# Kernel optimization log

Hardware: AMD Instinct MI355X
Metric: run time of the kernel (lower is better)

Reference implementation:

```python
import jax, jax.numpy as jnp
import numpy as np

D_MODEL = 1024
NUM_HEADS = 16
HEAD_DIM = D_MODEL // NUM_HEADS


def setup_inputs() -> dict:
    key = jax.random.key(0)
    ks = jax.random.split(key, 9)
    s = 1.0 / np.sqrt(D_MODEL)
    x = jax.random.normal(ks[0], (2, 2048, D_MODEL), dtype=jnp.float32)
    Wq = jax.random.normal(ks[1], (D_MODEL, D_MODEL), dtype=jnp.float32) * s
    Wk = jax.random.normal(ks[2], (D_MODEL, D_MODEL), dtype=jnp.float32) * s
    Wv = jax.random.normal(ks[3], (D_MODEL, D_MODEL), dtype=jnp.float32) * s
    Wo = jax.random.normal(ks[4], (D_MODEL, D_MODEL), dtype=jnp.float32) * s
    bq = jax.random.normal(ks[5], (D_MODEL,), dtype=jnp.float32) * s
    bk = jax.random.normal(ks[6], (D_MODEL,), dtype=jnp.float32) * s
    bv = jax.random.normal(ks[7], (D_MODEL,), dtype=jnp.float32) * s
    bo = jax.random.normal(ks[8], (D_MODEL,), dtype=jnp.float32) * s
    return {"x": x, "Wq": Wq, "bq": bq, "Wk": Wk, "bk": bk, "Wv": Wv, "bv": bv, "Wo": Wo, "bo": bo}


def reference(x, Wq, bq, Wk, bk, Wv, bv, Wo, bo):
    B, S, D = x.shape
    H, Hd = NUM_HEADS, HEAD_DIM
    # QKV projections
    q = (x @ Wq + bq).reshape(B, S, H, Hd).transpose(0, 2, 1, 3)  # [B,H,S,Hd]
    k = (x @ Wk + bk).reshape(B, S, H, Hd).transpose(0, 2, 1, 3)
    v = (x @ Wv + bv).reshape(B, S, H, Hd).transpose(0, 2, 1, 3)
    scores = jnp.einsum("bhqd,bhkd->bhqk", q, k) / jnp.sqrt(jnp.float32(Hd))
    attn = jax.nn.softmax(scores, axis=-1)
    out = jnp.einsum("bhqk,bhkd->bhqd", attn, v)  # [B,H,S,Hd]
    out = out.transpose(0, 2, 1, 3).reshape(B, S, D)
    return out @ Wo + bo
```

## Files before the change

kernel.cpp:

```cpp
#include <hip/hip_runtime.h>
#include <hip/hip_bf16.h>


typedef unsigned short u16;

#define D_MODEL 1024
#define NHEAD 16
#define HDIM 64
#define BATCH 2
#define SEQ 2048
#define MTOT (BATCH * SEQ)

#define QSCALE 0.18033688011112042f

using frag_ab = __attribute__((ext_vector_type(8))) short;
using frag_s4 = __attribute__((ext_vector_type(4))) short;
using frag_cd = __attribute__((ext_vector_type(4))) float;

__device__ __forceinline__ u16 f2u(float f) {
    union { float f; unsigned int i; } x;
    x.f = f;
    unsigned int r = x.i + 0x7fffu + ((x.i >> 16) & 1u);
    return (u16)(r >> 16);
}
__device__ __forceinline__ unsigned int pkrn(float a, float b) {
    union { __hip_bfloat162 h; unsigned int u; } c;
    c.h = __float22bfloat162_rn(float2{a, b});
    return c.u;
}

__global__ void prep(const float* __restrict__ W0, const float* __restrict__ W1,
                     const float* __restrict__ W2, const float* __restrict__ W3,
                     const float* __restrict__ X, u16* __restrict__ Wt,
                     u16* __restrict__ Xb) {
    const int z = blockIdx.z;
    const int tx = threadIdx.x, ty = threadIdx.y;
    if (z < 4) {
        __shared__ u16 t[32][33];
        const float* W = (z == 0) ? W0 : (z == 1) ? W1 : (z == 2) ? W2 : W3;
        u16* o = Wt + (size_t)z * D_MODEL * D_MODEL;
        int n0 = blockIdx.x * 32, k0 = blockIdx.y * 32;
        #pragma unroll
        for (int i = ty; i < 32; i += 8) t[i][tx] = f2u(W[(size_t)(k0 + i) * D_MODEL + n0 + tx]);
        __syncthreads();
        #pragma unroll
        for (int i = ty; i < 32; i += 8) o[(size_t)(n0 + i) * D_MODEL + k0 + tx] = t[tx][i];
    } else {
        int tid = ty * 32 + tx;
        size_t base = ((size_t)(blockIdx.y * 32 + blockIdx.x) * 256 + tid) * 16;
        #pragma unroll
        for (int c = 0; c < 4; ++c) {
            float4 v = *(const float4*)&X[base + c * 4];
            ushort4 o;
            o.x = f2u(v.x); o.y = f2u(v.y); o.z = f2u(v.z); o.w = f2u(v.w);
            *(ushort4*)&Xb[base + c * 4] = o;
        }
    }
}

__launch_bounds__(256, 3)
__global__ void gemm_qkvt(const u16* __restrict__ xb, const u16* __restrict__ Wt,
                          const float* __restrict__ bq, const float* __restrict__ bk,
                          const float* __restrict__ bv, u16* __restrict__ QKw,
                          u16* __restrict__ Vtw) {
    constexpr int BK = 64;
    __shared__ __attribute__((aligned(16))) u16 As[128 * BK];
    __shared__ __attribute__((aligned(16))) u16 Bs[128 * BK];

    const int tid = threadIdx.x;
    const int w = tid >> 6;
    const int lane = tid & 63;
    const int lrow = lane & 15, lquad = lane >> 4;
    const size_t WSZ = (size_t)D_MODEL * D_MODEL;

    const int bid = blockIdx.x;
    const bool vt = bid >= 512;
    const int z = vt ? 2 : (bid >> 8);
    const int t = vt ? (bid - 512) : (bid & 255);
    const int n0 = vt ? (t & 31) * 128 : (t & 7) * 128;
    const int m0 = vt ? (t >> 5) * 128 : (t >> 3) * 128;
    const u16* Ap = vt ? (Wt + 2 * WSZ) : xb;
    const u16* Bp = vt ? xb : (Wt + (size_t)z * WSZ);
    const float* bias = vt ? bv : (z ? bk : bq);

    frag_cd acc[4][4];
    #pragma unroll
    for (int i = 0; i < 4; i++)
        #pragma unroll
        for (int j = 0; j < 4; j++) acc[i][j] = (frag_cd){0.f, 0.f, 0.f, 0.f};

    const int wm = (w >> 1) * 64, wn = (w & 1) * 64;

    for (int k0 = 0; k0 < D_MODEL; k0 += BK) {
        __syncthreads();
        #pragma unroll
        for (int it = 0; it < 4; ++it) {
            int c = it * 256 + tid;
            int r = c >> 3, c8 = c & 7;
            const u16* ga = Ap + (size_t)(m0 + r) * D_MODEL + k0 + c8 * 8;
            char* la = (char*)As + (it * 256 + w * 64) * 16;
            __builtin_amdgcn_global_load_lds((const __attribute__((address_space(1))) void*)ga,
                                             (__attribute__((address_space(3))) void*)la, 16, 0, 0);
            const u16* gb = Bp + (size_t)(n0 + r) * D_MODEL + k0 + c8 * 8;
            char* lb = (char*)Bs + (it * 256 + w * 64) * 16;
            __builtin_amdgcn_global_load_lds((const __attribute__((address_space(1))) void*)gb,
                                             (__attribute__((address_space(3))) void*)lb, 16, 0, 0);
        }
        __syncthreads();

        #pragma unroll
        for (int kc = 0; kc < 2; ++kc) {
            frag_ab av[4], bvv[4];
            #pragma unroll
            for (int i = 0; i < 4; i++)
                av[i] = *(const frag_ab*)&As[(wm + i * 16 + lrow) * BK + kc * 32 + lquad * 8];
            #pragma unroll
            for (int j = 0; j < 4; j++)
                bvv[j] = *(const frag_ab*)&Bs[(wn + j * 16 + lrow) * BK + kc * 32 + lquad * 8];
            #pragma unroll
            for (int i = 0; i < 4; i++)
                #pragma unroll
                for (int j = 0; j < 4; j++)
                    acc[i][j] = __builtin_amdgcn_mfma_f32_16x16x32_bf16(av[i], bvv[j], acc[i][j], 0, 0, 0);
        }
    }

    const float scale = (!vt && z == 0) ? QSCALE : 1.0f;
    #pragma unroll
    for (int j = 0; j < 4; j++) {
        int gn = n0 + wn + j * 16 + lrow;
        #pragma unroll
        for (int i = 0; i < 4; i++) {
            #pragma unroll
            for (int rr = 0; rr < 4; ++rr) {
                int gm = m0 + wm + i * 16 + lquad * 4 + rr;
                if (!vt) {
                    float v = (acc[i][j][rr] + bias[gn]) * scale;
                    u16* oz = QKw + (size_t)z * ((size_t)MTOT * D_MODEL);
                    int b = gm >> 11, s = gm & (SEQ - 1);
                    int h = gn >> 6, d = gn & (HDIM - 1);
                    oz[(((size_t)(b * NHEAD + h)) * SEQ + s) * HDIM + d] = f2u(v);
                } else {
                    float v = acc[i][j][rr] + bias[gm];
                    int h = gm >> 6, d = gm & (HDIM - 1);
                    int b = gn >> 11, s = gn & (SEQ - 1);
                    Vtw[(((size_t)(b * NHEAD + h)) * HDIM + d) * SEQ + s] = f2u(v);
                }
            }
        }
    }
}

__launch_bounds__(256, 2)
__global__ void gemm_out(const u16* __restrict__ A, const u16* __restrict__ Wt,
                         const float* __restrict__ bias, float* __restrict__ out) {
    constexpr int BK = 64;
    __shared__ __attribute__((aligned(16))) u16 As[64 * BK];
    __shared__ __attribute__((aligned(16))) u16 Bs[128 * BK];

    const int tid = threadIdx.x;
    const int w = tid >> 6;
    const int lane = tid & 63;
    const int lrow = lane & 15, lquad = lane >> 4;
    const int m0 = blockIdx.y * 64, n0 = blockIdx.x * 128;

    frag_cd acc[2][4];
    #pragma unroll
    for (int i = 0; i < 2; i++)
        #pragma unroll
        for (int j = 0; j < 4; j++) acc[i][j] = (frag_cd){0.f, 0.f, 0.f, 0.f};

    const int wm = (w >> 1) * 32, wn = (w & 1) * 64;

    for (int k0 = 0; k0 < D_MODEL; k0 += BK) {
        __syncthreads();
        #pragma unroll
        for (int it = 0; it < 2; ++it) {
            int c = it * 256 + tid;
            int r = c >> 3, c8 = c & 7;
            const u16* ga = A + (size_t)(m0 + r) * D_MODEL + k0 + c8 * 8;
            char* la = (char*)As + (it * 256 + w * 64) * 16;
            __builtin_amdgcn_global_load_lds((const __attribute__((address_space(1))) void*)ga,
                                             (__attribute__((address_space(3))) void*)la, 16, 0, 0);
        }
        #pragma unroll
        for (int it = 0; it < 4; ++it) {
            int c = it * 256 + tid;
            int r = c >> 3, c8 = c & 7;
            const u16* gb = Wt + (size_t)(n0 + r) * D_MODEL + k0 + c8 * 8;
            char* lb = (char*)Bs + (it * 256 + w * 64) * 16;
            __builtin_amdgcn_global_load_lds((const __attribute__((address_space(1))) void*)gb,
                                             (__attribute__((address_space(3))) void*)lb, 16, 0, 0);
        }
        __syncthreads();

        #pragma unroll
        for (int kc = 0; kc < 2; ++kc) {
            frag_ab av[2], bvv[4];
            #pragma unroll
            for (int i = 0; i < 2; i++)
                av[i] = *(const frag_ab*)&As[(wm + i * 16 + lrow) * BK + kc * 32 + lquad * 8];
            #pragma unroll
            for (int j = 0; j < 4; j++)
                bvv[j] = *(const frag_ab*)&Bs[(wn + j * 16 + lrow) * BK + kc * 32 + lquad * 8];
            #pragma unroll
            for (int i = 0; i < 2; i++)
                #pragma unroll
                for (int j = 0; j < 4; j++)
                    acc[i][j] = __builtin_amdgcn_mfma_f32_16x16x32_bf16(av[i], bvv[j], acc[i][j], 0, 0, 0);
        }
    }

    #pragma unroll
    for (int j = 0; j < 4; j++) {
        int gn = n0 + wn + j * 16 + lrow;
        float bvf = bias[gn];
        #pragma unroll
        for (int i = 0; i < 2; i++)
            #pragma unroll
            for (int rr = 0; rr < 4; ++rr) {
                int gm = m0 + wm + i * 16 + lquad * 4 + rr;
                out[(size_t)gm * D_MODEL + gn] = acc[i][j][rr] + bvf;
            }
    }
}

__launch_bounds__(512, 4)
__global__ void attn_kernel(const u16* __restrict__ Q, const u16* __restrict__ K,
                            const u16* __restrict__ Vt, u16* __restrict__ O) {
    constexpr int SKK = 72;
    __shared__ __attribute__((aligned(16))) u16 Ks[128 * SKK];
    __shared__ __attribute__((aligned(16))) u16 Vs[64 * 128];

    const int tid = threadIdx.x;
    const int w = tid >> 6;
    const int lane = tid & 63;
    const int lrow = lane & 15, lquad = lane >> 4;
    const int bh = blockIdx.y;
    const int q0 = blockIdx.x * 128;
    const size_t base = (size_t)bh * SEQ * HDIM;
    const u16* Qg = Q + base;
    const u16* Kg = K + base;
    const u16* Vg = Vt + base;

    frag_ab qf[2];
    #pragma unroll
    for (int kc = 0; kc < 2; ++kc)
        qf[kc] = *(const frag_ab*)&Qg[(size_t)(q0 + w * 16 + lrow) * HDIM + kc * 32 + lquad * 8];

    frag_cd accOT[4];
    #pragma unroll
    for (int df = 0; df < 4; df++) accOT[df] = (frag_cd){0.f, 0.f, 0.f, 0.f};
    float lacc = 0.f;

    for (int kt = 0; kt < SEQ / 128; ++kt) {
        __syncthreads();
        #pragma unroll
        for (int it = 0; it < 2; ++it) {
            int c = it * 512 + tid;
            int rk = c >> 3, ck = (c & 7) * 8;
            *(uint4*)&Ks[rk * SKK + ck] = *(const uint4*)&Kg[(size_t)(kt * 128 + rk) * HDIM + ck];
            int rv = c >> 4, gv = c & 15;
            *(uint4*)&Vs[rv * 128 + ((gv ^ (rv & 7)) << 3)] =
                *(const uint4*)&Vg[(size_t)rv * SEQ + kt * 128 + gv * 8];
        }
        __syncthreads();

        frag_cd sc[8];
        #pragma unroll
        for (int mf = 0; mf < 8; mf++) sc[mf] = (frag_cd){0.f, 0.f, 0.f, 0.f};
        #pragma unroll
        for (int kc = 0; kc < 2; ++kc)
            #pragma unroll
            for (int mf = 0; mf < 8; mf++) {
                frag_ab kf = *(const frag_ab*)&Ks[(mf * 16 + lrow) * SKK + kc * 32 + lquad * 8];
                sc[mf] = __builtin_amdgcn_mfma_f32_16x16x32_bf16(kf, qf[kc], sc[mf], 0, 0, 0);
            }

        frag_s4 pk[8];
        #pragma unroll
        for (int mf = 0; mf < 8; mf++) {
            float e0 = exp2f(sc[mf][0]), e1 = exp2f(sc[mf][1]);
            float e2 = exp2f(sc[mf][2]), e3 = exp2f(sc[mf][3]);
            lacc += (e0 + e1) + (e2 + e3);
            union { frag_s4 s; unsigned int u[2]; } pu;
            pu.u[0] = pkrn(e0, e1);
            pu.u[1] = pkrn(e2, e3);
            pk[mf] = pu.s;
        }

        #pragma unroll
        for (int mf = 0; mf < 8; mf++)
            #pragma unroll
            for (int df = 0; df < 4; df++) {
                int dr = df * 16 + lrow;
                int g = 2 * mf + (lquad >> 1);
                frag_s4 vf = *(const frag_s4*)&Vs[dr * 128 + ((g ^ (dr & 7)) << 3) + (lquad & 1) * 4];
                accOT[df] = __builtin_amdgcn_mfma_f32_16x16x16bf16_1k(vf, pk[mf], accOT[df], 0, 0, 0);
            }
    }

    lacc += __shfl_xor(lacc, 16);
    lacc += __shfl_xor(lacc, 32);

    const int b = bh >> 4, h = bh & (NHEAD - 1);
    const int s = q0 + w * 16 + lrow;
    const float inv = 1.0f / lacc;
    u16* orow = O + ((size_t)(b * SEQ + s)) * D_MODEL + h * HDIM;
    #pragma unroll
    for (int df = 0; df < 4; df++) {
        union { unsigned int u[2]; ushort4 s4; } o;
        o.u[0] = pkrn(accOT[df][0] * inv, accOT[df][1] * inv);
        o.u[1] = pkrn(accOT[df][2] * inv, accOT[df][3] * inv);
        *(ushort4*)&orow[df * 16 + lquad * 4] = o.s4;
    }
}

extern "C" void kernel_launch(void* const* d_in, const int* in_sizes, int n_in,
                              void* d_out, int out_size, void* d_ws, size_t ws_size,
                              hipStream_t stream) {
    const float* x  = (const float*)d_in[0];
    const float* Wq = (const float*)d_in[1];
    const float* bq = (const float*)d_in[2];
    const float* Wk = (const float*)d_in[3];
    const float* bk = (const float*)d_in[4];
    const float* Wv = (const float*)d_in[5];
    const float* bv = (const float*)d_in[6];
    const float* Wo = (const float*)d_in[7];
    const float* bo = (const float*)d_in[8];

    u16* ws = (u16*)d_ws;
    const size_t WSZ = (size_t)D_MODEL * D_MODEL;
    const size_t TSZ = (size_t)MTOT * D_MODEL;
    u16* xb  = ws;
    u16* Wt  = ws + 4 * WSZ;
    u16* QKw = ws + 8 * WSZ;
    u16* Vtw = QKw + 2 * TSZ;
    u16* Aw  = Vtw + TSZ;

    prep<<<dim3(32, 32, 5), dim3(32, 8), 0, stream>>>(Wq, Wk, Wv, Wo, x, Wt, xb);
    gemm_qkvt<<<dim3(768), 256, 0, stream>>>(xb, Wt, bq, bk, bv, QKw, Vtw);
    attn_kernel<<<dim3(16, 32), 512, 0, stream>>>(QKw, QKw + TSZ, Vtw, Aw);
    gemm_out<<<dim3(8, 64), 256, 0, stream>>>(Aw, Wt + 3 * WSZ, bo, (float*)d_out);
}
```

Before: 220.4 us.

## Double-buffer K/V tiles in attention using async global-to-LDS loads

The attention kernel now keeps two LDS buffers for K and V. It prefetches the next key tile with direct global-to-LDS loads while the current tile feeds the MFMAs, and needs only one barrier per iteration instead of two. K moves from a padded layout to an XOR-swizzled layout so the direct-load lane mapping stays bank-conflict-free. The cost is doubled LDS per block (64KB), which may cut how many blocks fit on each CU.

```diff
diff --git a/kernel.cpp b/kernel.cpp
--- a/kernel.cpp
+++ b/kernel.cpp
@@ -228,9 +228,8 @@
 __launch_bounds__(512, 4)
 __global__ void attn_kernel(const u16* __restrict__ Q, const u16* __restrict__ K,
                             const u16* __restrict__ Vt, u16* __restrict__ O) {
-    constexpr int SKK = 72;
-    __shared__ __attribute__((aligned(16))) u16 Ks[128 * SKK];
-    __shared__ __attribute__((aligned(16))) u16 Vs[64 * 128];
+    __shared__ __attribute__((aligned(16))) u16 Ks[2][128 * 64];
+    __shared__ __attribute__((aligned(16))) u16 Vs[2][64 * 128];
 
     const int tid = threadIdx.x;
     const int w = tid >> 6;
@@ -253,29 +252,46 @@
     for (int df = 0; df < 4; df++) accOT[df] = (frag_cd){0.f, 0.f, 0.f, 0.f};
     float lacc = 0.f;
 
+    auto stage = [&](int bsel, int kt2) {
+        const u16* Kt = Kg + (size_t)(kt2 * 128) * HDIM;
+        #pragma unroll
+        for (int it = 0; it < 2; ++it) {
+            const int c = it * 512 + tid;
+            const int rk = c >> 3, ck = c & 7;
+            const u16* gk = Kt + rk * HDIM + ((ck ^ (rk & 7)) << 3);
+            char* lk = (char*)&Ks[bsel][0] + (it * 512 + w * 64) * 16;
+            __builtin_amdgcn_global_load_lds((const __attribute__((address_space(1))) void*)gk,
+                                             (__attribute__((address_space(3))) void*)lk, 16, 0, 0);
+            const int rv = c >> 4, gv = c & 15;
+            const u16* gvp = Vg + (size_t)rv * SEQ + kt2 * 128 + ((gv ^ (rv & 7)) << 3);
+            char* lv = (char*)&Vs[bsel][0] + (it * 512 + w * 64) * 16;
+            __builtin_amdgcn_global_load_lds((const __attribute__((address_space(1))) void*)gvp,
+                                             (__attribute__((address_space(3))) void*)lv, 16, 0, 0);
+        }
+    };
+
+    stage(0, 0);
+    __syncthreads();
+
+    int buf = 0;
     for (int kt = 0; kt < SEQ / 128; ++kt) {
-        __syncthreads();
-        #pragma unroll
-        for (int it = 0; it < 2; ++it) {
-            int c = it * 512 + tid;
-            int rk = c >> 3, ck = (c & 7) * 8;
-            *(uint4*)&Ks[rk * SKK + ck] = *(const uint4*)&Kg[(size_t)(kt * 128 + rk) * HDIM + ck];
-            int rv = c >> 4, gv = c & 15;
-            *(uint4*)&Vs[rv * 128 + ((gv ^ (rv & 7)) << 3)] =
-                *(const uint4*)&Vg[(size_t)rv * SEQ + kt * 128 + gv * 8];
-        }
-        __syncthreads();
+        if (kt + 1 < SEQ / 128) stage(buf ^ 1, kt + 1);
+
+        const u16* Ksb = &Ks[buf][0];
+        const u16* Vsb = &Vs[buf][0];
 
         frag_cd sc[8];
         #pragma unroll
         for (int mf = 0; mf < 8; mf++) sc[mf] = (frag_cd){0.f, 0.f, 0.f, 0.f};
         #pragma unroll
-        for (int kc = 0; kc < 2; ++kc)
+        for (int kc = 0; kc < 2; ++kc) {
+            const int cswz = (((kc << 2) + lquad) ^ (lrow & 7)) << 3;
             #pragma unroll
             for (int mf = 0; mf < 8; mf++) {
-                frag_ab kf = *(const frag_ab*)&Ks[(mf * 16 + lrow) * SKK + kc * 32 + lquad * 8];
+                frag_ab kf = *(const frag_ab*)&Ksb[(mf * 16 + lrow) * 64 + cswz];
                 sc[mf] = __builtin_amdgcn_mfma_f32_16x16x32_bf16(kf, qf[kc], sc[mf], 0, 0, 0);
             }
+        }
 
         frag_s4 pk[8];
         #pragma unroll
@@ -290,14 +306,18 @@
         }
 
         #pragma unroll
-        for (int mf = 0; mf < 8; mf++)
+        for (int mf = 0; mf < 8; mf++) {
+            const int g = 2 * mf + (lquad >> 1);
             #pragma unroll
             for (int df = 0; df < 4; df++) {
-                int dr = df * 16 + lrow;
-                int g = 2 * mf + (lquad >> 1);
-                frag_s4 vf = *(const frag_s4*)&Vs[dr * 128 + ((g ^ (dr & 7)) << 3) + (lquad & 1) * 4];
+                const int dr = df * 16 + lrow;
+                frag_s4 vf = *(const frag_s4*)&Vsb[dr * 128 + ((g ^ (lrow & 7)) << 3) + (lquad & 1) * 4];
                 accOT[df] = __builtin_amdgcn_mfma_f32_16x16x16bf16_1k(vf, pk[mf], accOT[df], 0, 0, 0);
             }
+        }
+
+        __syncthreads();
+        buf ^= 1;
     }
 
     lacc += __shfl_xor(lacc, 16);
```

After: 218.6 us. Within noise of the previous version (-0.8%).
